# Performance work log

Hardware: AMD Instinct MI355X
Metric: run time of the kernel (lower is better)

## Reference

```python
import jax, jax.numpy as jnp
import numpy as np

N_OBJ = 64      # number of components
M_PTS = 4_000_000  # total gaussians


def _quat_mul(a, b):
    # Hamilton product, wxyz convention: a (.., 4) x b (.., 4) -> (.., 4)
    aw, ax, ay, az = a[..., 0], a[..., 1], a[..., 2], a[..., 3]
    bw, bx, by, bz = b[..., 0], b[..., 1], b[..., 2], b[..., 3]
    return jnp.stack([
        aw * bw - ax * bx - ay * by - az * bz,
        aw * bx + ax * bw + ay * bz - az * by,
        aw * by - ax * bz + ay * bw + az * bx,
        aw * bz + ax * by - ay * bx + az * bw,
    ], axis=-1)


def _quat_rotate(q, v):
    # Rotate vectors v (.., 3) by quaternions q (.., 4), wxyz: v' = v + w*t + q_xyz x t, t = 2 q_xyz x v
    w = q[..., 0:1]
    xyz = q[..., 1:4]
    t = 2.0 * jnp.cross(xyz, v)
    return v + w * t + jnp.cross(xyz, t)


def setup_inputs() -> dict:
    key = jax.random.key(0)
    k1, k2, k3, k4, k5 = jax.random.split(key, 5)
    trans = jax.random.normal(k1, (N_OBJ, 3), dtype=jnp.float32)
    rotors = jax.random.normal(k2, (N_OBJ, 4), dtype=jnp.float32)
    rotors = rotors / jnp.linalg.norm(rotors, axis=-1, keepdims=True)  # unit rotors
    means = jax.random.normal(k3, (M_PTS, 3), dtype=jnp.float32)
    quats = jax.random.normal(k4, (M_PTS, 4), dtype=jnp.float32)
    indices = jax.random.randint(k5, (M_PTS,), 0, N_OBJ, dtype=jnp.int32)
    return {"trans": trans, "rotors": rotors, "means": means, "quats": quats, "indices": indices}


def reference(trans, rotors, means, quats, indices):
    # Gather per-point rigid transform of the owning component
    t = trans[indices]    # (m, 3)
    r = rotors[indices]   # (m, 4)
    result_means = _quat_rotate(r, means) + t   # rotate then translate
    result_quats = _quat_mul(r, quats)          # compose orientations
    return result_means, result_quats
```

## Files before the change

### kernel.cpp

```cpp
#include <hip/hip_runtime.h>

typedef float f4 __attribute__((ext_vector_type(4)));
typedef int   i4 __attribute__((ext_vector_type(4)));

#define NOBJ 64

__global__ __launch_bounds__(256) void compose_kernel(
    const float* __restrict__ trans,
    const float* __restrict__ rotors,
    const float* __restrict__ means,
    const float* __restrict__ quats,
    const int*   __restrict__ indices,
    float* __restrict__ out,
    int M)
{
    __shared__ f4 s_obj[NOBJ][2];
    const int tid = threadIdx.x;
    if (tid < NOBJ) {
        s_obj[tid][0] = ((const f4*)rotors)[tid];
        f4 tr;
        tr.x = trans[tid * 3 + 0];
        tr.y = trans[tid * 3 + 1];
        tr.z = trans[tid * 3 + 2];
        tr.w = 0.0f;
        s_obj[tid][1] = tr;
    }
    __syncthreads();

    float* out_means = out;
    float* out_quats = out + (size_t)M * 3;

    const int nquads  = M >> 2;
    const int gstride = gridDim.x * blockDim.x;

    for (int t = blockIdx.x * blockDim.x + tid; t < nquads; t += gstride) {
        f4 m0 = ((const f4*)means)[t * 3 + 0];
        f4 m1 = ((const f4*)means)[t * 3 + 1];
        f4 m2 = ((const f4*)means)[t * 3 + 2];
        f4 qin0 = ((const f4*)quats)[t * 4 + 0];
        f4 qin1 = ((const f4*)quats)[t * 4 + 1];
        f4 qin2 = ((const f4*)quats)[t * 4 + 2];
        f4 qin3 = ((const f4*)quats)[t * 4 + 3];
        i4 idx = ((const i4*)indices)[t];

        const float vx[4] = {m0.x, m0.w, m1.z, m2.y};
        const float vy[4] = {m0.y, m1.x, m1.w, m2.z};
        const float vz[4] = {m0.z, m1.y, m2.x, m2.w};
        const f4 qin[4] = {qin0, qin1, qin2, qin3};

        float om[12];
        f4 oq[4];

#pragma unroll
        for (int p = 0; p < 4; ++p) {
            const int id = idx[p];
            const f4 r  = s_obj[id][0];
            const f4 tr = s_obj[id][1];
            const float rw = r.x, rx = r.y, ry = r.z, rz = r.w;

            const float t2x = 2.0f * (ry * vz[p] - rz * vy[p]);
            const float t2y = 2.0f * (rz * vx[p] - rx * vz[p]);
            const float t2z = 2.0f * (rx * vy[p] - ry * vx[p]);
            om[p * 3 + 0] = vx[p] + rw * t2x + (ry * t2z - rz * t2y) + tr.x;
            om[p * 3 + 1] = vy[p] + rw * t2y + (rz * t2x - rx * t2z) + tr.y;
            om[p * 3 + 2] = vz[p] + rw * t2z + (rx * t2y - ry * t2x) + tr.z;

            const float bw = qin[p].x, bx = qin[p].y, by = qin[p].z, bz = qin[p].w;
            f4 o;
            o.x = rw * bw - rx * bx - ry * by - rz * bz;
            o.y = rw * bx + rx * bw + ry * bz - rz * by;
            o.z = rw * by - rx * bz + ry * bw + rz * bx;
            o.w = rw * bz + rx * by - ry * bx + rz * bw;
            oq[p] = o;
        }

        f4 s0 = {om[0], om[1], om[2],  om[3]};
        f4 s1 = {om[4], om[5], om[6],  om[7]};
        f4 s2 = {om[8], om[9], om[10], om[11]};
        ((f4*)out_means)[t * 3 + 0] = s0;
        ((f4*)out_means)[t * 3 + 1] = s1;
        ((f4*)out_means)[t * 3 + 2] = s2;
        ((f4*)out_quats)[t * 4 + 0] = oq[0];
        ((f4*)out_quats)[t * 4 + 1] = oq[1];
        ((f4*)out_quats)[t * 4 + 2] = oq[2];
        ((f4*)out_quats)[t * 4 + 3] = oq[3];
    }

    const int tail = M & 3;
    if (tail) {
        const int g = blockIdx.x * blockDim.x + tid;
        if (g < tail) {
            const int i  = nquads * 4 + g;
            const int id = indices[i];
            const f4 r  = s_obj[id][0];
            const f4 tr = s_obj[id][1];
            const float rw = r.x, rx = r.y, ry = r.z, rz = r.w;
            const float vx_ = means[i * 3 + 0];
            const float vy_ = means[i * 3 + 1];
            const float vz_ = means[i * 3 + 2];
            const float t2x = 2.0f * (ry * vz_ - rz * vy_);
            const float t2y = 2.0f * (rz * vx_ - rx * vz_);
            const float t2z = 2.0f * (rx * vy_ - ry * vx_);
            out_means[i * 3 + 0] = vx_ + rw * t2x + (ry * t2z - rz * t2y) + tr.x;
            out_means[i * 3 + 1] = vy_ + rw * t2y + (rz * t2x - rx * t2z) + tr.y;
            out_means[i * 3 + 2] = vz_ + rw * t2z + (rx * t2y - ry * t2x) + tr.z;
            const float bw = quats[i * 4 + 0], bx = quats[i * 4 + 1];
            const float by = quats[i * 4 + 2], bz = quats[i * 4 + 3];
            out_quats[i * 4 + 0] = rw * bw - rx * bx - ry * by - rz * bz;
            out_quats[i * 4 + 1] = rw * bx + rx * bw + ry * bz - rz * by;
            out_quats[i * 4 + 2] = rw * by - rx * bz + ry * bw + rz * bx;
            out_quats[i * 4 + 3] = rw * bz + rx * by - ry * bx + rz * bw;
        }
    }
}

extern "C" void kernel_launch(void* const* d_in, const int* in_sizes, int n_in,
                              void* d_out, int out_size, void* d_ws, size_t ws_size,
                              hipStream_t stream) {
    const float* trans   = (const float*)d_in[0];
    const float* rotors  = (const float*)d_in[1];
    const float* means   = (const float*)d_in[2];
    const float* quats   = (const float*)d_in[3];
    const int*   indices = (const int*)d_in[4];
    const int M = in_sizes[4];
    float* out = (float*)d_out;

    const int threads = 256;
    int nquads = M >> 2;
    if (nquads < 1) nquads = 1;
    int blocks = (nquads + threads - 1) / threads;

    compose_kernel<<<blocks, threads, 0, stream>>>(trans, rotors, means, quats,
                                                   indices, out, M);
}
```

Baseline: 49.74 us.

## Process eight points per thread, SoA shared table, nontemporal stores

Each thread now handles eight points instead of four, issuing more 16-byte loads per thread so more memory requests are in flight. The per-object table in shared memory moves from an array of float4 pairs to a structure of arrays with seven scalar rows, which changes the LDS access pattern from two 16-byte reads to seven 4-byte reads. Outputs are written with nontemporal stores to avoid polluting cache with streaming data. The grid is halved to match, which raises register pressure and lowers the number of waves in flight.

```diff
diff --git a/kernel.cpp b/kernel.cpp
--- a/kernel.cpp
+++ b/kernel.cpp
@@ -4,6 +4,7 @@
 typedef int   i4 __attribute__((ext_vector_type(4)));
 
 #define NOBJ 64
+#define PPT  8
 
 __global__ __launch_bounds__(256) void compose_kernel(
     const float* __restrict__ trans,
@@ -14,96 +15,95 @@
     float* __restrict__ out,
     int M)
 {
-    __shared__ f4 s_obj[NOBJ][2];
+    __shared__ float s_tab[7][NOBJ];
     const int tid = threadIdx.x;
     if (tid < NOBJ) {
-        s_obj[tid][0] = ((const f4*)rotors)[tid];
-        f4 tr;
-        tr.x = trans[tid * 3 + 0];
-        tr.y = trans[tid * 3 + 1];
-        tr.z = trans[tid * 3 + 2];
-        tr.w = 0.0f;
-        s_obj[tid][1] = tr;
+        f4 r = ((const f4*)rotors)[tid];
+        s_tab[0][tid] = r.x;
+        s_tab[1][tid] = r.y;
+        s_tab[2][tid] = r.z;
+        s_tab[3][tid] = r.w;
+        s_tab[4][tid] = trans[tid * 3 + 0];
+        s_tab[5][tid] = trans[tid * 3 + 1];
+        s_tab[6][tid] = trans[tid * 3 + 2];
     }
     __syncthreads();
 
     float* out_means = out;
     float* out_quats = out + (size_t)M * 3;
 
-    const int nquads  = M >> 2;
+    const int ngroups = M >> 3;
     const int gstride = gridDim.x * blockDim.x;
 
-    for (int t = blockIdx.x * blockDim.x + tid; t < nquads; t += gstride) {
-        f4 m0 = ((const f4*)means)[t * 3 + 0];
-        f4 m1 = ((const f4*)means)[t * 3 + 1];
-        f4 m2 = ((const f4*)means)[t * 3 + 2];
-        f4 qin0 = ((const f4*)quats)[t * 4 + 0];
-        f4 qin1 = ((const f4*)quats)[t * 4 + 1];
-        f4 qin2 = ((const f4*)quats)[t * 4 + 2];
-        f4 qin3 = ((const f4*)quats)[t * 4 + 3];
-        i4 idx = ((const i4*)indices)[t];
+    for (int t = blockIdx.x * blockDim.x + tid; t < ngroups; t += gstride) {
+        f4 mv[6];
+#pragma unroll
+        for (int k = 0; k < 6; ++k) mv[k] = ((const f4*)means)[t * 6 + k];
+        f4 qv[8];
+#pragma unroll
+        for (int k = 0; k < 8; ++k) qv[k] = ((const f4*)quats)[t * 8 + k];
+        i4 ia = ((const i4*)indices)[t * 2 + 0];
+        i4 ib = ((const i4*)indices)[t * 2 + 1];
 
-        const float vx[4] = {m0.x, m0.w, m1.z, m2.y};
-        const float vy[4] = {m0.y, m1.x, m1.w, m2.z};
-        const float vz[4] = {m0.z, m1.y, m2.x, m2.w};
-        const f4 qin[4] = {qin0, qin1, qin2, qin3};
-
-        float om[12];
-        f4 oq[4];
+        f4 sm[6];
+        f4 sq[8];
 
 #pragma unroll
-        for (int p = 0; p < 4; ++p) {
-            const int id = idx[p];
-            const f4 r  = s_obj[id][0];
-            const f4 tr = s_obj[id][1];
-            const float rw = r.x, rx = r.y, ry = r.z, rz = r.w;
+        for (int p = 0; p < 8; ++p) {
+            const int id = (p < 4) ? ia[p] : ib[p - 4];
+            const float rw = s_tab[0][id];
+            const float rx = s_tab[1][id];
+            const float ry = s_tab[2][id];
+            const float rz = s_tab[3][id];
+            const float tx = s_tab[4][id];
+            const float ty = s_tab[5][id];
+            const float tz = s_tab[6][id];
 
-            const float t2x = 2.0f * (ry * vz[p] - rz * vy[p]);
-            const float t2y = 2.0f * (rz * vx[p] - rx * vz[p]);
-            const float t2z = 2.0f * (rx * vy[p] - ry * vx[p]);
-            om[p * 3 + 0] = vx[p] + rw * t2x + (ry * t2z - rz * t2y) + tr.x;
-            om[p * 3 + 1] = vy[p] + rw * t2y + (rz * t2x - rx * t2z) + tr.y;
-            om[p * 3 + 2] = vz[p] + rw * t2z + (rx * t2y - ry * t2x) + tr.z;
+            const float vx = mv[(3 * p + 0) >> 2][(3 * p + 0) & 3];
+            const float vy = mv[(3 * p + 1) >> 2][(3 * p + 1) & 3];
+            const float vz = mv[(3 * p + 2) >> 2][(3 * p + 2) & 3];
 
-            const float bw = qin[p].x, bx = qin[p].y, by = qin[p].z, bz = qin[p].w;
+            const float t2x = 2.0f * (ry * vz - rz * vy);
+            const float t2y = 2.0f * (rz * vx - rx * vz);
+            const float t2z = 2.0f * (rx * vy - ry * vx);
+            sm[(3 * p + 0) >> 2][(3 * p + 0) & 3] = vx + rw * t2x + (ry * t2z - rz * t2y) + tx;
+            sm[(3 * p + 1) >> 2][(3 * p + 1) & 3] = vy + rw * t2y + (rz * t2x - rx * t2z) + ty;
+            sm[(3 * p + 2) >> 2][(3 * p + 2) & 3] = vz + rw * t2z + (rx * t2y - ry * t2x) + tz;
+
+            const float bw = qv[p].x, bx = qv[p].y, by = qv[p].z, bz = qv[p].w;
             f4 o;
             o.x = rw * bw - rx * bx - ry * by - rz * bz;
             o.y = rw * bx + rx * bw + ry * bz - rz * by;
             o.z = rw * by - rx * bz + ry * bw + rz * bx;
             o.w = rw * bz + rx * by - ry * bx + rz * bw;
-            oq[p] = o;
+            sq[p] = o;
         }
 
-        f4 s0 = {om[0], om[1], om[2],  om[3]};
-        f4 s1 = {om[4], om[5], om[6],  om[7]};
-        f4 s2 = {om[8], om[9], om[10], om[11]};
-        ((f4*)out_means)[t * 3 + 0] = s0;
-        ((f4*)out_means)[t * 3 + 1] = s1;
-        ((f4*)out_means)[t * 3 + 2] = s2;
-        ((f4*)out_quats)[t * 4 + 0] = oq[0];
-        ((f4*)out_quats)[t * 4 + 1] = oq[1];
-        ((f4*)out_quats)[t * 4 + 2] = oq[2];
-        ((f4*)out_quats)[t * 4 + 3] = oq[3];
+#pragma unroll
+        for (int k = 0; k < 6; ++k)
+            __builtin_nontemporal_store(sm[k], &((f4*)out_means)[t * 6 + k]);
+#pragma unroll
+        for (int k = 0; k < 8; ++k)
+            __builtin_nontemporal_store(sq[k], &((f4*)out_quats)[t * 8 + k]);
     }
 
-    const int tail = M & 3;
+    const int tail = M & 7;
     if (tail) {
         const int g = blockIdx.x * blockDim.x + tid;
         if (g < tail) {
-            const int i  = nquads * 4 + g;
+            const int i  = (M >> 3) * 8 + g;
             const int id = indices[i];
-            const f4 r  = s_obj[id][0];
-            const f4 tr = s_obj[id][1];
-            const float rw = r.x, rx = r.y, ry = r.z, rz = r.w;
+            const float rw = s_tab[0][id], rx = s_tab[1][id];
+            const float ry = s_tab[2][id], rz = s_tab[3][id];
             const float vx_ = means[i * 3 + 0];
             const float vy_ = means[i * 3 + 1];
             const float vz_ = means[i * 3 + 2];
             const float t2x = 2.0f * (ry * vz_ - rz * vy_);
             const float t2y = 2.0f * (rz * vx_ - rx * vz_);
             const float t2z = 2.0f * (rx * vy_ - ry * vx_);
-            out_means[i * 3 + 0] = vx_ + rw * t2x + (ry * t2z - rz * t2y) + tr.x;
-            out_means[i * 3 + 1] = vy_ + rw * t2y + (rz * t2x - rx * t2z) + tr.y;
-            out_means[i * 3 + 2] = vz_ + rw * t2z + (rx * t2y - ry * t2x) + tr.z;
+            out_means[i * 3 + 0] = vx_ + rw * t2x + (ry * t2z - rz * t2y) + s_tab[4][id];
+            out_means[i * 3 + 1] = vy_ + rw * t2y + (rz * t2x - rx * t2z) + s_tab[5][id];
+            out_means[i * 3 + 2] = vz_ + rw * t2z + (rx * t2y - ry * t2x) + s_tab[6][id];
             const float bw = quats[i * 4 + 0], bx = quats[i * 4 + 1];
             const float by = quats[i * 4 + 2], bz = quats[i * 4 + 3];
             out_quats[i * 4 + 0] = rw * bw - rx * bx - ry * by - rz * bz;
@@ -126,9 +126,9 @@
     float* out = (float*)d_out;
 
     const int threads = 256;
-    int nquads = M >> 2;
-    if (nquads < 1) nquads = 1;
-    int blocks = (nquads + threads - 1) / threads;
+    int ngroups = M >> 3;
+    if (ngroups < 1) ngroups = 1;
+    int blocks = (ngroups + threads - 1) / threads;
 
     compose_kernel<<<blocks, threads, 0, stream>>>(trans, rotors, means, quats,
                                                    indices, out, M);
```

Measured after the change: 184.9 us. +271.8%, slower.
